# Kernel optimization log

Measured on AMD Instinct MI355X. Metric: run time of the kernel, lower is better.

The kernel has to match this reference:

```python
import jax, jax.numpy as jnp
import numpy as np

NG, NL, NCAM, NP, ED = 8, 4, 6, 7, 256  # groups, levels, cams, key points, embed dims
GD = ED // NG
FIX_SCALE = jnp.array([[0.0, 0.0, 0.0], [0.45, 0.0, 0.0], [-0.45, 0.0, 0.0],
                       [0.0, 0.45, 0.0], [0.0, -0.45, 0.0], [0.0, 0.0, 0.45],
                       [0.0, 0.0, -0.45]], dtype=jnp.float32)


def grid_sample_bilinear(feat, grid):
    """feat [N,C,H,W], grid [N,A,P,2] in [-1,1]; bilinear, zeros padding, align_corners=False."""
    N, C, H, W = feat.shape
    A, P = grid.shape[1], grid.shape[2]
    gx = (grid[..., 0] + 1.0) * (W * 0.5) - 0.5
    gy = (grid[..., 1] + 1.0) * (H * 0.5) - 0.5
    x0 = jnp.floor(gx)
    y0 = jnp.floor(gy)
    wx1 = gx - x0
    wy1 = gy - y0
    feat_flat = feat.reshape(N, C, H * W)

    def gather(xi, yi, w):
        valid = (xi >= 0) & (xi <= W - 1) & (yi >= 0) & (yi <= H - 1)
        xc = jnp.clip(xi, 0, W - 1).astype(jnp.int32)
        yc = jnp.clip(yi, 0, H - 1).astype(jnp.int32)
        idx = (yc * W + xc).reshape(N, 1, A * P)
        vals = jnp.take_along_axis(feat_flat, idx, axis=2)  # [N,C,A*P]
        return vals * (w * valid).reshape(N, 1, A * P)

    out = (gather(x0, y0, (1.0 - wx1) * (1.0 - wy1))
           + gather(x0 + 1.0, y0, wx1 * (1.0 - wy1))
           + gather(x0, y0 + 1.0, (1.0 - wx1) * wy1)
           + gather(x0 + 1.0, y0 + 1.0, wx1 * wy1))
    return out.reshape(N, C, A, P)


def _forward(instance_feature, anchor, anchor_embed, feat0, feat1, feat2, feat3,
             projection_mat, image_wh, w_fc, b_fc, w_out, b_out):
    B, A = anchor.shape[:2]
    # --- key point generation (box_code_size=8: size + yaw rotation + translation) ---
    size = jnp.exp(anchor[..., 3:6])[:, :, None, :]           # [B,A,1,3]
    kp = FIX_SCALE * size                                      # [B,A,7,3]
    sin, cos = anchor[..., 6], anchor[..., 7]
    z = jnp.zeros_like(cos)
    o = jnp.ones_like(cos)
    rot = jnp.stack([jnp.stack([cos, -sin, z], -1),
                     jnp.stack([sin, cos, z], -1),
                     jnp.stack([z, z, o], -1)], -2)            # [B,A,3,3]
    kp = jnp.einsum('baij,bapj->bapi', rot, kp) + anchor[..., None, 0:3]

    # --- attention weights: softmax over cams*levels*pts per group ---
    feature = instance_feature + anchor_embed
    w = feature @ w_fc.T + b_fc                                # [B,A,NG*NCAM*NL*NP]
    w = jax.nn.softmax(w.reshape(B, A, NCAM * NL * NP, NG), axis=2)
    w = w.reshape(B, A, NCAM, NL, NP, NG)

    # --- project key points to normalized image coords ---
    pts = jnp.concatenate([kp, jnp.ones_like(kp[..., :1])], -1)  # [B,A,7,4]
    p2d = jnp.einsum('bcij,bapj->bcapi', projection_mat, pts)[..., :3]
    xy = p2d[..., :2] / jnp.maximum(p2d[..., 2:3], 1e-5)
    xy = xy / jnp.maximum(image_wh[:, :, None, None], 1e-5)
    grid = (xy * 2.0 - 1.0).reshape(B * NCAM, A, NP, 2)

    # --- multilevel bilinear sampling ---
    levels = [feat0, feat1, feat2, feat3]
    sampled = jnp.stack([grid_sample_bilinear(f.reshape((B * NCAM,) + f.shape[2:]), grid)
                         for f in levels], axis=1)             # [B*Ncam,NL,C,A,P]
    feats = sampled.reshape(B, NCAM, NL, ED, A, NP).transpose(0, 4, 1, 2, 5, 3)  # [B,A,Ncam,NL,P,C]
    feats = feats.reshape(B, A, NCAM, NL, NP, NG, GD)

    # --- weighted fusion over cams, levels, then sum over key points ---
    fused = jnp.einsum('bacnpgd,bacnpg->bagd', feats, w).reshape(B, A, ED)
    return fused @ w_out.T + b_out


def setup_inputs() -> dict:
    ks = jax.random.split(jax.random.key(0), 13)
    B, A = 2, 900
    return {
        'instance_feature': jax.random.normal(ks[0], (B, A, ED), jnp.float32),
        'anchor': jax.random.normal(ks[1], (B, A, 8), jnp.float32),
        'anchor_embed': jax.random.normal(ks[2], (B, A, ED), jnp.float32),
        'feat0': jax.random.normal(ks[3], (B, NCAM, ED, 64, 176), jnp.float32),
        'feat1': jax.random.normal(ks[4], (B, NCAM, ED, 32, 88), jnp.float32),
        'feat2': jax.random.normal(ks[5], (B, NCAM, ED, 16, 44), jnp.float32),
        'feat3': jax.random.normal(ks[6], (B, NCAM, ED, 8, 22), jnp.float32),
        'projection_mat': jax.random.normal(ks[7], (B, NCAM, 4, 4), jnp.float32),
        'image_wh': jnp.ones((B, NCAM, 2), jnp.float32),
        'w_fc': jax.random.normal(ks[8], (NG * NCAM * NL * NP, ED), jnp.float32) * 0.02,
        'b_fc': jax.random.normal(ks[9], (NG * NCAM * NL * NP,), jnp.float32) * 0.02,
        'w_out': jax.random.normal(ks[10], (ED, ED), jnp.float32) * 0.02,
        'b_out': jax.random.normal(ks[11], (ED,), jnp.float32) * 0.02,
    }


def reference(instance_feature, anchor, anchor_embed, feat0, feat1, feat2, feat3,
              projection_mat, image_wh, w_fc, b_fc, w_out, b_out):
    return _forward(instance_feature, anchor, anchor_embed, feat0, feat1, feat2, feat3,
                    projection_mat, image_wh, w_fc, b_fc, w_out, b_out)
```

## Files before the change

### kernel.cpp

```cpp
#include <hip/hip_runtime.h>
#include <math.h>

constexpr int B = 2, A = 900, ED = 256, NG = 8, NCAM = 6, NL = 4, NP = 7;
constexpr int NJ = NG * NCAM * NL * NP;
constexpr int NBA = B * A;
constexpr int NE = NCAM * NL * NP;
constexpr int SPLIT = 2;
constexpr int EHALF = NE / SPLIT;
constexpr int TPB = 231;

__constant__ float FIXS[NP][3] = {
  {0.f,0.f,0.f},{0.45f,0.f,0.f},{-0.45f,0.f,0.f},
  {0.f,0.45f,0.f},{0.f,-0.45f,0.f},{0.f,0.f,0.45f},{0.f,0.f,-0.45f}};

__constant__ int cH[NL]  = {64,32,16,8};
__constant__ int cW[NL]  = {176,88,44,22};
__constant__ int cHW[NL] = {11264,2816,704,176};
__constant__ long long cLOFF[NL] = {0LL, 0LL, 8650752LL, 10813440LL};

__global__ __launch_bounds__(256) void k_tr_cl(
    const float* __restrict__ f1, const float* __restrict__ f2,
    const float* __restrict__ f3, float* __restrict__ tfeat)
{
  __shared__ float smem[64 * 65];
  const int bc = blockIdx.y;
  const int bx = blockIdx.x;
  const int t  = threadIdx.x;

  int lvl, px0, ch0;
  const float* src;
  if (bx < 176)      { lvl = 1; src = f1; px0 = (bx >> 2) * 64;         ch0 = (bx & 3) * 64; }
  else if (bx < 220) { lvl = 2; src = f2; px0 = ((bx - 176) >> 2) * 64; ch0 = ((bx - 176) & 3) * 64; }
  else               { lvl = 3; src = f3; px0 = (bx - 220) * 16;        ch0 = 0; }
  const int HW = cHW[lvl];
  const float* in = src + (size_t)bc * ED * HW;
  float* outp = tfeat + cLOFF[lvl] + (size_t)bc * HW * ED;

  if (lvl < 3) {
    const int pxl = t & 15, cr = t >> 4;
#pragma unroll
    for (int i = 0; i < 4; ++i) {
      const int ch = cr + 16*i;
      const float4 v = *(const float4*)(in + (size_t)(ch0 + ch)*HW + px0 + 4*pxl);
      smem[(4*pxl+0)*65 + ch] = v.x;
      smem[(4*pxl+1)*65 + ch] = v.y;
      smem[(4*pxl+2)*65 + ch] = v.z;
      smem[(4*pxl+3)*65 + ch] = v.w;
    }
    __syncthreads();
    const int chl = t & 15, pw = t >> 4;
#pragma unroll
    for (int i = 0; i < 4; ++i) {
      const int px = pw + 16*i;
      float4 v;
      v.x = smem[px*65 + 4*chl + 0];
      v.y = smem[px*65 + 4*chl + 1];
      v.z = smem[px*65 + 4*chl + 2];
      v.w = smem[px*65 + 4*chl + 3];
      *(float4*)(outp + (size_t)(px0 + px)*ED + ch0 + 4*chl) = v;
    }
  } else {
    const int pxl = t & 3, cr = t >> 2;
#pragma unroll
    for (int i = 0; i < 4; ++i) {
      const int ch = cr + 64*i;
      const float4 v = *(const float4*)(in + (size_t)ch*HW + px0 + 4*pxl);
      smem[(4*pxl+0)*257 + ch] = v.x;
      smem[(4*pxl+1)*257 + ch] = v.y;
      smem[(4*pxl+2)*257 + ch] = v.z;
      smem[(4*pxl+3)*257 + ch] = v.w;
    }
    __syncthreads();
    const int chl = t & 63, pw = t >> 6;
#pragma unroll
    for (int i = 0; i < 4; ++i) {
      const int px = pw + 4*i;
      float4 v;
      v.x = smem[px*257 + 4*chl + 0];
      v.y = smem[px*257 + 4*chl + 1];
      v.z = smem[px*257 + 4*chl + 2];
      v.w = smem[px*257 + 4*chl + 3];
      *(float4*)(outp + (size_t)(px0 + px)*ED + 4*chl) = v;
    }
  }
}

__global__ __launch_bounds__(256) void k_tr(const float* __restrict__ in,
                                            float* __restrict__ out, int R, int C)
{
  __shared__ float tile[32][33];
  const int r0 = blockIdx.y * 32, c0 = blockIdx.x * 32;
  const int tx = threadIdx.x, ty = threadIdx.y;
#pragma unroll
  for (int kk = 0; kk < 4; ++kk) {
    const int r = r0 + ty + kk*8, c = c0 + tx;
    if (r < R && c < C) tile[ty + kk*8][tx] = in[(size_t)r*C + c];
  }
  __syncthreads();
#pragma unroll
  for (int kk = 0; kk < 4; ++kk) {
    const int c = c0 + ty + kk*8, r = r0 + tx;
    if (r < R && c < C) out[(size_t)c*R + r] = tile[tx][ty + kk*8];
  }
}

__global__ __launch_bounds__(192) void k_fc(const float* __restrict__ inst,
    const float* __restrict__ emb, const float* __restrict__ wt,
    const float* __restrict__ b_fc, float* __restrict__ wraw)
{
  __shared__ float fsh[8][ED];
  const int a0 = blockIdx.x * 8;
  const int j  = blockIdx.y * 192 + threadIdx.x;
  const int t  = threadIdx.x;

  for (int i = t; i < 8 * ED; i += 192) {
    const int a = i >> 8, k = i & 255;
    const size_t idx = (size_t)(a0 + a) * ED + k;
    fsh[a][k] = inst[idx] + emb[idx];
  }
  __syncthreads();

  float acc[8] = {0.f,0.f,0.f,0.f,0.f,0.f,0.f,0.f};
  for (int k = 0; k < ED; k += 4) {
    float w0 = wt[(size_t)(k+0)*NJ + j];
    float w1 = wt[(size_t)(k+1)*NJ + j];
    float w2 = wt[(size_t)(k+2)*NJ + j];
    float w3 = wt[(size_t)(k+3)*NJ + j];
#pragma unroll
    for (int a = 0; a < 8; ++a)
      acc[a] += w0*fsh[a][k] + w1*fsh[a][k+1] + w2*fsh[a][k+2] + w3*fsh[a][k+3];
  }
  const float bj = b_fc[j];
#pragma unroll
  for (int a = 0; a < 8; ++a)
    wraw[(size_t)(a0+a)*NJ + j] = acc[a] + bj;
}

template<bool CL>
__global__ __launch_bounds__(256) void k_sample_h(
    const float* __restrict__ anchor, const float* __restrict__ proj,
    const float* __restrict__ wh, const float* __restrict__ wraw,
    const float* __restrict__ tfeat,
    const float* __restrict__ f0, const float* __restrict__ f1,
    const float* __restrict__ f2, const float* __restrict__ f3,
    float* __restrict__ fused)
{
  __shared__ float wsh[NJ];
  __shared__ float gridsh[NCAM][NP][2];
  __shared__ const float* cptr[EHALF][4];
  __shared__ float4 cwt[EHALF];
  __shared__ int2   cmeta[EHALF];
  __shared__ int wcnt[4];

  const int ba   = blockIdx.x;
  const int half = blockIdx.y;
  const int b    = ba / A;
  const int t    = threadIdx.x;

  for (int j = t; j < NJ; j += 256)
    wsh[(j & 7) * NE + (j >> 3)] = wraw[(size_t)ba*NJ + j];

  if (t < NCAM*NP) {
    const int c = t / NP, p = t % NP;
    const float* an = anchor + (size_t)ba * 8;
    const float sx = expf(an[3]), sy = expf(an[4]), sz = expf(an[5]);
    const float sn = an[6], cs = an[7];
    const float kx = FIXS[p][0]*sx, ky = FIXS[p][1]*sy, kz = FIXS[p][2]*sz;
    const float px = cs*kx - sn*ky + an[0];
    const float py = sn*kx + cs*ky + an[1];
    const float pz = kz + an[2];
    const float* P = proj + ((size_t)(b*NCAM + c))*16;
    const float X = P[0]*px + P[1]*py + P[2]*pz  + P[3];
    const float Y = P[4]*px + P[5]*py + P[6]*pz  + P[7];
    const float Z = P[8]*px + P[9]*py + P[10]*pz + P[11];
    const float zc  = fmaxf(Z, 1e-5f);
    const float whx = fmaxf(wh[(b*NCAM+c)*2+0], 1e-5f);
    const float why = fmaxf(wh[(b*NCAM+c)*2+1], 1e-5f);
    gridsh[c][p][0] = (X/zc/whx)*2.f - 1.f;
    gridsh[c][p][1] = (Y/zc/why)*2.f - 1.f;
  }
  __syncthreads();

  bool valid = false;
  int chstep = 0;
  float4 w4 = make_float4(0.f,0.f,0.f,0.f);
  const float *p00=nullptr, *p10=nullptr, *p01=nullptr, *p11=nullptr;
  const int e = half * EHALF + t;
  if (t < EHALF) {
    const int c = e / (NL*NP); const int r = e % (NL*NP);
    const int l = r / NP, p = r % NP;
    const int Wl = cW[l], Hl = cH[l], HWl = cHW[l];
    const float gx = (gridsh[c][p][0] + 1.f) * (Wl * 0.5f) - 0.5f;
    const float gy = (gridsh[c][p][1] + 1.f) * (Hl * 0.5f) - 0.5f;
    const float x0f = floorf(gx), y0f = floorf(gy);
    const bool vx0 = (x0f >=  0.f) & (x0f <= (float)(Wl-1));
    const bool vx1 = (x0f >= -1.f) & (x0f <= (float)(Wl-2));
    const bool vy0 = (y0f >=  0.f) & (y0f <= (float)(Hl-1));
    const bool vy1 = (y0f >= -1.f) & (y0f <= (float)(Hl-2));
    if (vx0|vx1|vy0|vy1) {
      const float wx1 = gx - x0f, wy1 = gy - y0f;
      const int x0 = (int)fmaxf(fminf(x0f,        (float)(Wl-1)), 0.f);
      const int x1 = (int)fmaxf(fminf(x0f + 1.f,  (float)(Wl-1)), 0.f);
      const int y0 = (int)fmaxf(fminf(y0f,        (float)(Hl-1)), 0.f);
      const int y1 = (int)fmaxf(fminf(y0f + 1.f,  (float)(Hl-1)), 0.f);
      w4 = make_float4((1.f-wx1)*(1.f-wy1)*(vx0&&vy0),
                       wx1*(1.f-wy1)*(vx1&&vy0),
                       (1.f-wx1)*wy1*(vx0&&vy1),
                       wx1*wy1*(vx1&&vy1));
      if (w4.x != 0.f || w4.y != 0.f || w4.z != 0.f || w4.w != 0.f) {
        const float* base;
        int estep;
        if (CL && l >= 1) {
          base = tfeat + cLOFF[l] + (size_t)(b*NCAM + c) * HWl * ED;
          estep = ED; chstep = 1;
        } else {
          const float* fp = (l==0)?f0:(l==1)?f1:(l==2)?f2:f3;
          base = fp + (size_t)(b*NCAM + c) * ED * HWl;
          estep = 1; chstep = HWl;
        }
        p00 = base + (size_t)(y0*Wl + x0) * estep;
        p10 = base + (size_t)(y0*Wl + x1) * estep;
        p01 = base + (size_t)(y1*Wl + x0) * estep;
        p11 = base + (size_t)(y1*Wl + x1) * estep;
        valid = true;
      }
    }
  }

  const unsigned long long mask = __ballot(valid);
  const int lane = t & 63, wv = t >> 6;
  if (lane == 0) wcnt[wv] = __popcll(mask);
  __syncthreads();
  int off = 0, nv = 0;
#pragma unroll
  for (int i = 0; i < 4; ++i) { if (i < wv) off += wcnt[i]; nv += wcnt[i]; }
  if (valid) {
    const int pos = off + __popcll(mask & ((1ull << lane) - 1ull));
    cptr[pos][0] = p00; cptr[pos][1] = p10; cptr[pos][2] = p01; cptr[pos][3] = p11;
    cwt[pos]   = w4;
    cmeta[pos] = make_int2(chstep, e);
  }

  {
    const int g = t >> 5, ln = t & 31;
    float* wg = wsh + g * NE;
    float m = -3.4e38f;
    for (int i = ln; i < NE; i += 32) m = fmaxf(m, wg[i]);
#pragma unroll
    for (int mk = 16; mk >= 1; mk >>= 1) m = fmaxf(m, __shfl_xor(m, mk));
    float s = 0.f;
    for (int i = ln; i < NE; i += 32) {
      const float ev = expf(wg[i] - m);
      wg[i] = ev;
      s += ev;
    }
#pragma unroll
    for (int mk = 16; mk >= 1; mk >>= 1) s += __shfl_xor(s, mk);
    const float inv = 1.f / s;
    for (int i = ln; i < NE; i += 32) wg[i] *= inv;
  }
  __syncthreads();

  float acc = 0.f;
  const int g = t >> 5;
#pragma unroll 4
  for (int i = 0; i < nv; ++i) {
    const int2 m = cmeta[i];
    const size_t toff = (size_t)t * m.x;
    const float4 w = cwt[i];
    const float aw = wsh[g*NE + m.y];
    const float v00 = cptr[i][0][toff];
    const float v10 = cptr[i][1][toff];
    const float v01 = cptr[i][2][toff];
    const float v11 = cptr[i][3][toff];
    acc += aw * (w.x*v00 + w.y*v10 + w.z*v01 + w.w*v11);
  }
  fused[((size_t)half * NBA + ba) * ED + t] = acc;
}

__global__ __launch_bounds__(256) void k_out(const float* __restrict__ fused,
    const float* __restrict__ w_out, const float* __restrict__ b_out,
    float* __restrict__ out)
{
  __shared__ float fsh[8][ED];
  const int a0 = blockIdx.x * 8;
  const int t = threadIdx.x;
#pragma unroll
  for (int k = 0; k < 8; ++k)
    fsh[k][t] = fused[(size_t)(a0+k)*ED + t]
              + fused[(size_t)NBA*ED + (size_t)(a0+k)*ED + t];
  __syncthreads();
  float acc[8] = {0.f,0.f,0.f,0.f,0.f,0.f,0.f,0.f};
  for (int i = 0; i < ED; i += 4) {
    const float4 w4 = *(const float4*)&w_out[(size_t)t*ED + i];
#pragma unroll
    for (int k = 0; k < 8; ++k) {
      const float4 fv = *(const float4*)&fsh[k][i];
      acc[k] += w4.x*fv.x + w4.y*fv.y + w4.z*fv.z + w4.w*fv.w;
    }
  }
  const float bo = b_out[t];
#pragma unroll
  for (int k = 0; k < 8; ++k) out[(size_t)(a0+k)*ED + t] = acc[k] + bo;
}

extern "C" void kernel_launch(void* const* d_in, const int* in_sizes, int n_in,
                              void* d_out, int out_size, void* d_ws, size_t ws_size,
                              hipStream_t stream) {
  const float* inst   = (const float*)d_in[0];
  const float* anchor = (const float*)d_in[1];
  const float* emb    = (const float*)d_in[2];
  const float* f0 = (const float*)d_in[3];
  const float* f1 = (const float*)d_in[4];
  const float* f2 = (const float*)d_in[5];
  const float* f3 = (const float*)d_in[6];
  const float* proj  = (const float*)d_in[7];
  const float* wh    = (const float*)d_in[8];
  const float* w_fc  = (const float*)d_in[9];
  const float* b_fc  = (const float*)d_in[10];
  const float* w_out = (const float*)d_in[11];
  const float* b_out = (const float*)d_in[12];
  float* out = (float*)d_out;
  float* ws  = (float*)d_ws;

  const size_t TFEAT = 11354112ULL;
  const size_t WRAW  = (size_t)NBA * NJ;
  const size_t FUSED = (size_t)SPLIT * NBA * ED;
  const size_t WT    = (size_t)ED * NJ;
  const bool tr = ws_size >= (TFEAT + WRAW + FUSED + WT) * sizeof(float);

  float* tfeat  = ws;
  float* wraw   = tr ? (ws + TFEAT) : ws;
  float* fusedp = wraw + WRAW;
  float* wt     = fusedp + FUSED;

  k_tr<<<dim3(ED/32, NJ/32, 1), dim3(32,8), 0, stream>>>(w_fc, wt, NJ, ED);

  if (tr)
    k_tr_cl<<<dim3(TPB, B*NCAM), 256, 0, stream>>>(f1, f2, f3, tfeat);

  k_fc<<<dim3(NBA / 8, 7), 192, 0, stream>>>(inst, emb, wt, b_fc, wraw);

  if (tr)
    k_sample_h<true><<<dim3(NBA, SPLIT), 256, 0, stream>>>(anchor, proj, wh,
        wraw, tfeat, f0, f1, f2, f3, fusedp);
  else
    k_sample_h<false><<<dim3(NBA, SPLIT), 256, 0, stream>>>(anchor, proj, wh,
        wraw, tfeat, f0, f1, f2, f3, fusedp);

  k_out<<<NBA / 8, 256, 0, stream>>>(fusedp, w_out, b_out, out);
}
```

Baseline: 352.9 us.

## Fuse output projection into sampler, drop split, merge transpose kernels

```diff
diff --git a/kernel.cpp b/kernel.cpp
--- a/kernel.cpp
+++ b/kernel.cpp
@@ -5,9 +5,10 @@
 constexpr int NJ = NG * NCAM * NL * NP;
 constexpr int NBA = B * A;
 constexpr int NE = NCAM * NL * NP;
-constexpr int SPLIT = 2;
-constexpr int EHALF = NE / SPLIT;
-constexpr int TPB = 231;
+
+constexpr int NWFB = 336;
+constexpr int TPB  = 231;
+constexpr int NTRB = TPB * B * NCAM;
 
 __constant__ float FIXS[NP][3] = {
   {0.f,0.f,0.f},{0.45f,0.f,0.f},{-0.45f,0.f,0.f},
@@ -18,15 +19,31 @@
 __constant__ int cHW[NL] = {11264,2816,704,176};
 __constant__ long long cLOFF[NL] = {0LL, 0LL, 8650752LL, 10813440LL};
 
-__global__ __launch_bounds__(256) void k_tr_cl(
+__global__ __launch_bounds__(256) void k_prep_tr(
     const float* __restrict__ f1, const float* __restrict__ f2,
-    const float* __restrict__ f3, float* __restrict__ tfeat)
+    const float* __restrict__ f3, const float* __restrict__ w_fc,
+    float* __restrict__ tfeat, float* __restrict__ wt)
 {
   __shared__ float smem[64 * 65];
-  const int bc = blockIdx.y;
-  const int bx = blockIdx.x;
-  const int t  = threadIdx.x;
-
+  const int bid = blockIdx.x;
+  const int t   = threadIdx.x;
+
+  if (bid < NWFB) {
+    const int r0 = (bid >> 3) * 32, c0 = (bid & 7) * 32;
+    const int tx = t & 31, ty = t >> 5;
+#pragma unroll
+    for (int i = 0; i < 4; ++i)
+      smem[(ty + 8*i)*33 + tx] = w_fc[(size_t)(r0 + ty + 8*i)*ED + c0 + tx];
+    __syncthreads();
+#pragma unroll
+    for (int i = 0; i < 4; ++i)
+      wt[(size_t)(c0 + ty + 8*i)*NJ + r0 + tx] = smem[tx*33 + ty + 8*i];
+    return;
+  }
+
+  const int fb = bid - NWFB;
+  const int bc = fb / TPB;
+  const int bx = fb % TPB;
   int lvl, px0, ch0;
   const float* src;
   if (bx < 176)      { lvl = 1; src = f1; px0 = (bx >> 2) * 64;         ch0 = (bx & 3) * 64; }
@@ -85,25 +102,6 @@
   }
 }
 
-__global__ __launch_bounds__(256) void k_tr(const float* __restrict__ in,
-                                            float* __restrict__ out, int R, int C)
-{
-  __shared__ float tile[32][33];
-  const int r0 = blockIdx.y * 32, c0 = blockIdx.x * 32;
-  const int tx = threadIdx.x, ty = threadIdx.y;
-#pragma unroll
-  for (int kk = 0; kk < 4; ++kk) {
-    const int r = r0 + ty + kk*8, c = c0 + tx;
-    if (r < R && c < C) tile[ty + kk*8][tx] = in[(size_t)r*C + c];
-  }
-  __syncthreads();
-#pragma unroll
-  for (int kk = 0; kk < 4; ++kk) {
-    const int c = c0 + ty + kk*8, r = r0 + tx;
-    if (r < R && c < C) out[(size_t)c*R + r] = tile[tx][ty + kk*8];
-  }
-}
-
 __global__ __launch_bounds__(192) void k_fc(const float* __restrict__ inst,
     const float* __restrict__ emb, const float* __restrict__ wt,
     const float* __restrict__ b_fc, float* __restrict__ wraw)
@@ -137,25 +135,26 @@
 }
 
 template<bool CL>
-__global__ __launch_bounds__(256) void k_sample_h(
+__global__ __launch_bounds__(256) void k_sample_o(
     const float* __restrict__ anchor, const float* __restrict__ proj,
     const float* __restrict__ wh, const float* __restrict__ wraw,
     const float* __restrict__ tfeat,
     const float* __restrict__ f0, const float* __restrict__ f1,
     const float* __restrict__ f2, const float* __restrict__ f3,
-    float* __restrict__ fused)
+    const float* __restrict__ w_out, const float* __restrict__ b_out,
+    float* __restrict__ out)
 {
   __shared__ float wsh[NJ];
   __shared__ float gridsh[NCAM][NP][2];
-  __shared__ const float* cptr[EHALF][4];
-  __shared__ float4 cwt[EHALF];
-  __shared__ int2   cmeta[EHALF];
+  __shared__ const float* cptr[NE][4];
+  __shared__ float4 cwt[NE];
+  __shared__ int2   cmeta[NE];
   __shared__ int wcnt[4];
-
-  const int ba   = blockIdx.x;
-  const int half = blockIdx.y;
-  const int b    = ba / A;
-  const int t    = threadIdx.x;
+  __shared__ float fused_sh[ED];
+
+  const int ba = blockIdx.x;
+  const int b  = ba / A;
+  const int t  = threadIdx.x;
 
   for (int j = t; j < NJ; j += 256)
     wsh[(j & 7) * NE + (j >> 3)] = wraw[(size_t)ba*NJ + j];
@@ -185,8 +184,8 @@
   int chstep = 0;
   float4 w4 = make_float4(0.f,0.f,0.f,0.f);
   const float *p00=nullptr, *p10=nullptr, *p01=nullptr, *p11=nullptr;
-  const int e = half * EHALF + t;
-  if (t < EHALF) {
+  if (t < NE) {
+    const int e = t;
     const int c = e / (NL*NP); const int r = e % (NL*NP);
     const int l = r / NP, p = r % NP;
     const int Wl = cW[l], Hl = cH[l], HWl = cHW[l];
@@ -238,7 +237,7 @@
     const int pos = off + __popcll(mask & ((1ull << lane) - 1ull));
     cptr[pos][0] = p00; cptr[pos][1] = p10; cptr[pos][2] = p01; cptr[pos][3] = p11;
     cwt[pos]   = w4;
-    cmeta[pos] = make_int2(chstep, e);
+    cmeta[pos] = make_int2(chstep, t);
   }
 
   {
@@ -275,33 +274,16 @@
     const float v11 = cptr[i][3][toff];
     acc += aw * (w.x*v00 + w.y*v10 + w.z*v01 + w.w*v11);
   }
-  fused[((size_t)half * NBA + ba) * ED + t] = acc;
-}
-
-__global__ __launch_bounds__(256) void k_out(const float* __restrict__ fused,
-    const float* __restrict__ w_out, const float* __restrict__ b_out,
-    float* __restrict__ out)
-{
-  __shared__ float fsh[8][ED];
-  const int a0 = blockIdx.x * 8;
-  const int t = threadIdx.x;
-#pragma unroll
-  for (int k = 0; k < 8; ++k)
-    fsh[k][t] = fused[(size_t)(a0+k)*ED + t]
-              + fused[(size_t)NBA*ED + (size_t)(a0+k)*ED + t];
-  __syncthreads();
-  float acc[8] = {0.f,0.f,0.f,0.f,0.f,0.f,0.f,0.f};
+  fused_sh[t] = acc;
+  __syncthreads();
+
+  float o = 0.f;
   for (int i = 0; i < ED; i += 4) {
-    const float4 w4 = *(const float4*)&w_out[(size_t)t*ED + i];
-#pragma unroll
-    for (int k = 0; k < 8; ++k) {
-      const float4 fv = *(const float4*)&fsh[k][i];
-      acc[k] += w4.x*fv.x + w4.y*fv.y + w4.z*fv.z + w4.w*fv.w;
-    }
-  }
-  const float bo = b_out[t];
-#pragma unroll
-  for (int k = 0; k < 8; ++k) out[(size_t)(a0+k)*ED + t] = acc[k] + bo;
+    const float4 wv4 = *(const float4*)&w_out[(size_t)t*ED + i];
+    const float4 fv  = *(const float4*)&fused_sh[i];
+    o += wv4.x*fv.x + wv4.y*fv.y + wv4.z*fv.z + wv4.w*fv.w;
+  }
+  out[(size_t)ba*ED + t] = o + b_out[t];
 }
 
 extern "C" void kernel_launch(void* const* d_in, const int* in_sizes, int n_in,
@@ -325,28 +307,22 @@
 
   const size_t TFEAT = 11354112ULL;
   const size_t WRAW  = (size_t)NBA * NJ;
-  const size_t FUSED = (size_t)SPLIT * NBA * ED;
   const size_t WT    = (size_t)ED * NJ;
-  const bool tr = ws_size >= (TFEAT + WRAW + FUSED + WT) * sizeof(float);
-
-  float* tfeat  = ws;
-  float* wraw   = tr ? (ws + TFEAT) : ws;
-  float* fusedp = wraw + WRAW;
-  float* wt     = fusedp + FUSED;
-
-  k_tr<<<dim3(ED/32, NJ/32, 1), dim3(32,8), 0, stream>>>(w_fc, wt, NJ, ED);
+  const bool tr = ws_size >= (TFEAT + WRAW + WT) * sizeof(float);
+
+  float* tfeat = ws;
+  float* wraw  = tr ? (ws + TFEAT) : ws;
+  float* wt    = wraw + WRAW;
+
+  k_prep_tr<<<NWFB + (tr ? NTRB : 0), 256, 0, stream>>>(f1, f2, f3, w_fc,
+                                                        tfeat, wt);
+
+  k_fc<<<dim3(NBA / 8, 7), 192, 0, stream>>>(inst, emb, wt, b_fc, wraw);
 
   if (tr)
-    k_tr_cl<<<dim3(TPB, B*NCAM), 256, 0, stream>>>(f1, f2, f3, tfeat);
-
-  k_fc<<<dim3(NBA / 8, 7), 192, 0, stream>>>(inst, emb, wt, b_fc, wraw);
-
-  if (tr)
-    k_sample_h<true><<<dim3(NBA, SPLIT), 256, 0, stream>>>(anchor, proj, wh,
-        wraw, tfeat, f0, f1, f2, f3, fusedp);
+    k_sample_o<true><<<NBA, 256, 0, stream>>>(anchor, proj, wh, wraw, tfeat,
+        f0, f1, f2, f3, w_out, b_out, out);
   else
-    k_sample_h<false><<<dim3(NBA, SPLIT), 256, 0, stream>>>(anchor, proj, wh,
-        wraw, tfeat, f0, f1, f2, f3, fusedp);
-
-  k_out<<<NBA / 8, 256, 0, stream>>>(fusedp, w_out, b_out, out);
+    k_sample_o<false><<<NBA, 256, 0, stream>>>(anchor, proj, wh, wraw, tfeat,
+        f0, f1, f2, f3, w_out, b_out, out);
 }
```

Result: slower. 372.2 us (+5.5%).
